# Kernel tuning notes

Measured on AMD Instinct MI355X. Metric: run time of the kernel, lower is better.

Reference implementation:

```python
import jax, jax.numpy as jnp
import numpy as np

B, H, W, C = 1, 56, 56, 96
DI = 192          # d_inner = ssm_ratio * hidden_dim
N  = 16           # d_state
DR = 6            # dt_rank = ceil(96/16)
K  = 4            # cross-scan directions
MH = 384          # mlp hidden = 4*C
L  = H * W


def _ln(x, g, b):
    m = x.mean(-1, keepdims=True)
    v = ((x - m) ** 2).mean(-1, keepdims=True)
    return (x - m) * jax.lax.rsqrt(v + 1e-5) * g + b


def setup_inputs() -> dict:
    key = jax.random.key(0)
    ks = jax.random.split(key, 12)
    r = lambda i, shape, s=0.02: jax.random.normal(ks[i], shape, jnp.float32) * s
    # S4D-real init for A_logs: log(1..N) tiled over K*DI channels
    A_logs = jnp.log(jnp.tile(jnp.arange(1, N + 1, dtype=jnp.float32)[None, :], (K * DI, 1)))
    return dict(
        x=jax.random.normal(ks[0], (B, H, W, C), jnp.float32),
        norm_g=jnp.ones((C,)), norm_b=jnp.zeros((C,)),
        in_proj_w=r(1, (C, 2 * DI)),
        conv_w=r(2, (3, 3, 1, DI)), conv_b=jnp.zeros((DI,)),
        x_proj_w=r(3, (K, DR + 2 * N, DI)),
        dt_projs_w=r(4, (K, DI, DR), 0.1), dt_projs_b=r(5, (K, DI), 0.1),
        A_logs=A_logs, Ds=jnp.ones((K * DI,)),
        out_norm_g=jnp.ones((DI,)), out_norm_b=jnp.zeros((DI,)),
        out_proj_w=r(6, (DI, C)),
        norm2_g=jnp.ones((C,)), norm2_b=jnp.zeros((C,)),
        fc1_w=r(7, (C, MH)), fc1_b=jnp.zeros((MH,)),
        fc2_w=r(8, (MH, C)), fc2_b=jnp.zeros((C,)),
    )


def _ss2d(x, in_proj_w, conv_w, conv_b, x_proj_w, dt_projs_w, dt_projs_b,
          A_logs, Ds, out_norm_g, out_norm_b, out_proj_w):
    xz = x @ in_proj_w                                  # (B,H,W,2*DI)
    xx, z = xz[..., :DI], xz[..., DI:]
    z = jax.nn.silu(z)
    xx = jax.lax.conv_general_dilated(
        xx, conv_w, (1, 1), 'SAME',
        dimension_numbers=('NHWC', 'HWIO', 'NHWC'),
        feature_group_count=DI) + conv_b               # depthwise 3x3
    xx = jax.nn.silu(xx)
    # cross-scan: row-major, col-major, and their reverses -> (B,K,DI,L)
    xd = jnp.transpose(xx, (0, 3, 1, 2)).reshape(B, DI, L)
    xt = jnp.transpose(xx, (0, 3, 2, 1)).reshape(B, DI, L)
    xs = jnp.stack([xd, xt, xd[..., ::-1], xt[..., ::-1]], 1)
    xdbl = jnp.einsum('bkdl,kcd->bkcl', xs, x_proj_w)
    dts, Bs, Cs = xdbl[:, :, :DR], xdbl[:, :, DR:DR + N], xdbl[:, :, DR + N:]
    dts = jnp.einsum('bkrl,kdr->bkdl', dts, dt_projs_w)
    dts = jax.nn.softplus(dts + dt_projs_b[None, :, :, None])      # (B,K,DI,L)
    A = -jnp.exp(A_logs).reshape(K, DI, N)
    # selective scan as first-order linear recurrence h_t = a_t*h_{t-1} + b_t
    a = jnp.exp(dts[..., None] * A[None, :, :, None, :])           # (B,K,DI,L,N)
    b = dts[..., None] * jnp.swapaxes(Bs, -1, -2)[:, :, None] * xs[..., None]
    def comb(c1, c2):
        a1, b1 = c1
        a2, b2 = c2
        return a1 * a2, a2 * b1 + b2
    _, hs = jax.lax.associative_scan(comb, (a, b), axis=3)         # (B,K,DI,L,N)
    ys = jnp.einsum('bkdln,bknl->bkdl', hs, Cs) + Ds.reshape(K, DI)[None, :, :, None] * xs
    # cross-merge: un-flip, un-transpose, sum the 4 directions
    yrow = ys[:, 0] + ys[:, 2, :, ::-1]
    ycol = ys[:, 1] + ys[:, 3, :, ::-1]
    y = yrow + jnp.transpose(ycol.reshape(B, DI, W, H), (0, 1, 3, 2)).reshape(B, DI, L)
    y = jnp.transpose(y.reshape(B, DI, H, W), (0, 2, 3, 1))        # (B,H,W,DI)
    y = _ln(y, out_norm_g, out_norm_b) * z
    return y @ out_proj_w


def reference(x, norm_g, norm_b, in_proj_w, conv_w, conv_b, x_proj_w,
              dt_projs_w, dt_projs_b, A_logs, Ds, out_norm_g, out_norm_b,
              out_proj_w, norm2_g, norm2_b, fc1_w, fc1_b, fc2_w, fc2_b):
    x = x + _ss2d(_ln(x, norm_g, norm_b), in_proj_w, conv_w, conv_b, x_proj_w,
                  dt_projs_w, dt_projs_b, A_logs, Ds, out_norm_g, out_norm_b, out_proj_w)
    h = _ln(x, norm2_g, norm2_b)
    x = x + (jax.nn.gelu(h @ fc1_w + fc1_b) @ fc2_w + fc2_b)
    return x
```

## Files before the change

kernel.cpp:

```cpp
#include <hip/hip_runtime.h>
#include <math.h>

constexpr int cH = 56, cW = 56, cC = 96, cDI = 192, cN = 16, cDR = 6, cK = 4, cMH = 384;
constexpr int cL = cH * cW;
constexpr int cNC = 196;
constexpr int cCH = 16;
constexpr float LOG2E = 1.44269504088896340736f;

__device__ __forceinline__ float fast_exp2(float x) { return __builtin_amdgcn_exp2f(x); }
__device__ __forceinline__ float siluf(float x) { return x / (1.f + expf(-x)); }
__device__ __forceinline__ float geluf(float x) {
    float x3 = x * x * x;
    return 0.5f * x * (1.f + tanhf(0.7978845608028654f * (x + 0.044715f * x3)));
}

__global__ void ln96_kernel(const float* __restrict__ x, const float* __restrict__ g,
                            const float* __restrict__ b, float* __restrict__ out, int M) {
    int wid = threadIdx.x >> 6;
    int lane = threadIdx.x & 63;
    int row = blockIdx.x * 4 + wid;
    if (row >= M) return;
    const float* xr = x + row * cC;
    float v0 = xr[lane];
    float v1 = (lane < cC - 64) ? xr[lane + 64] : 0.f;
    float s = v0 + v1;
    float sq = v0 * v0 + v1 * v1;
#pragma unroll
    for (int off = 32; off; off >>= 1) {
        s += __shfl_xor(s, off, 64);
        sq += __shfl_xor(sq, off, 64);
    }
    float m = s * (1.f / cC);
    float var = sq * (1.f / cC) - m * m;
    float rstd = rsqrtf(var + 1e-5f);
    out[row * cC + lane] = (v0 - m) * rstd * g[lane] + b[lane];
    if (lane < cC - 64)
        out[row * cC + lane + 64] = (v1 - m) * rstd * g[lane + 64] + b[lane + 64];
}

template <int ACT, bool HASB, bool HASR>
__global__ __launch_bounds__(256) void gemm_tile_kernel(
    const float* __restrict__ A, const float* __restrict__ B,
    const float* __restrict__ bias, const float* __restrict__ res,
    float* __restrict__ C, int M, int Nn, int Kk) {
    __shared__ float As[64][36];
    __shared__ float Bs[32][32];
    int tid = threadIdx.x;
    int tx = tid & 15;
    int ty = tid >> 4;
    int row0 = blockIdx.y * 64;
    int n0 = blockIdx.x * 32;
    float acc[4][2] = {{0.f, 0.f}, {0.f, 0.f}, {0.f, 0.f}, {0.f, 0.f}};
    int nt = Kk >> 5;
    for (int kt = 0; kt < nt; kt++) {
#pragma unroll
        for (int t = 0; t < 2; t++) {
            int f = tid + t * 256;
            int ar = f >> 3, ac = (f & 7) * 4;
            const float4 v = *reinterpret_cast<const float4*>(
                A + (size_t)(row0 + ar) * Kk + kt * 32 + ac);
            *reinterpret_cast<float4*>(&As[ar][ac]) = v;
        }
        {
            int br = tid >> 3, bc = (tid & 7) * 4;
            const float4 v = *reinterpret_cast<const float4*>(
                B + (size_t)(kt * 32 + br) * Nn + n0 + bc);
            *reinterpret_cast<float4*>(&Bs[br][bc]) = v;
        }
        __syncthreads();
#pragma unroll
        for (int k4 = 0; k4 < 8; k4++) {
            float4 a0 = *reinterpret_cast<float4*>(&As[ty * 4 + 0][k4 * 4]);
            float4 a1 = *reinterpret_cast<float4*>(&As[ty * 4 + 1][k4 * 4]);
            float4 a2 = *reinterpret_cast<float4*>(&As[ty * 4 + 2][k4 * 4]);
            float4 a3 = *reinterpret_cast<float4*>(&As[ty * 4 + 3][k4 * 4]);
            float2 b0 = *reinterpret_cast<float2*>(&Bs[k4 * 4 + 0][tx * 2]);
            float2 b1 = *reinterpret_cast<float2*>(&Bs[k4 * 4 + 1][tx * 2]);
            float2 b2 = *reinterpret_cast<float2*>(&Bs[k4 * 4 + 2][tx * 2]);
            float2 b3 = *reinterpret_cast<float2*>(&Bs[k4 * 4 + 3][tx * 2]);
            acc[0][0] = fmaf(a0.x, b0.x, acc[0][0]); acc[0][1] = fmaf(a0.x, b0.y, acc[0][1]);
            acc[1][0] = fmaf(a1.x, b0.x, acc[1][0]); acc[1][1] = fmaf(a1.x, b0.y, acc[1][1]);
            acc[2][0] = fmaf(a2.x, b0.x, acc[2][0]); acc[2][1] = fmaf(a2.x, b0.y, acc[2][1]);
            acc[3][0] = fmaf(a3.x, b0.x, acc[3][0]); acc[3][1] = fmaf(a3.x, b0.y, acc[3][1]);
            acc[0][0] = fmaf(a0.y, b1.x, acc[0][0]); acc[0][1] = fmaf(a0.y, b1.y, acc[0][1]);
            acc[1][0] = fmaf(a1.y, b1.x, acc[1][0]); acc[1][1] = fmaf(a1.y, b1.y, acc[1][1]);
            acc[2][0] = fmaf(a2.y, b1.x, acc[2][0]); acc[2][1] = fmaf(a2.y, b1.y, acc[2][1]);
            acc[3][0] = fmaf(a3.y, b1.x, acc[3][0]); acc[3][1] = fmaf(a3.y, b1.y, acc[3][1]);
            acc[0][0] = fmaf(a0.z, b2.x, acc[0][0]); acc[0][1] = fmaf(a0.z, b2.y, acc[0][1]);
            acc[1][0] = fmaf(a1.z, b2.x, acc[1][0]); acc[1][1] = fmaf(a1.z, b2.y, acc[1][1]);
            acc[2][0] = fmaf(a2.z, b2.x, acc[2][0]); acc[2][1] = fmaf(a2.z, b2.y, acc[2][1]);
            acc[3][0] = fmaf(a3.z, b2.x, acc[3][0]); acc[3][1] = fmaf(a3.z, b2.y, acc[3][1]);
            acc[0][0] = fmaf(a0.w, b3.x, acc[0][0]); acc[0][1] = fmaf(a0.w, b3.y, acc[0][1]);
            acc[1][0] = fmaf(a1.w, b3.x, acc[1][0]); acc[1][1] = fmaf(a1.w, b3.y, acc[1][1]);
            acc[2][0] = fmaf(a2.w, b3.x, acc[2][0]); acc[2][1] = fmaf(a2.w, b3.y, acc[2][1]);
            acc[3][0] = fmaf(a3.w, b3.x, acc[3][0]); acc[3][1] = fmaf(a3.w, b3.y, acc[3][1]);
        }
        __syncthreads();
    }
    int cc = n0 + tx * 2;
    float bx_ = 0.f, by_ = 0.f;
    if (HASB) { bx_ = bias[cc]; by_ = bias[cc + 1]; }
#pragma unroll
    for (int i = 0; i < 4; i++) {
        int rr = row0 + ty * 4 + i;
        float v0 = acc[i][0], v1 = acc[i][1];
        if (HASB) { v0 += bx_; v1 += by_; }
        if (ACT == 1) { v0 = geluf(v0); v1 = geluf(v1); }
        if (HASR) {
            const float2 r2 = *reinterpret_cast<const float2*>(res + (size_t)rr * Nn + cc);
            v0 += r2.x; v1 += r2.y;
        }
        float2 o; o.x = v0; o.y = v1;
        *reinterpret_cast<float2*>(C + (size_t)rr * Nn + cc) = o;
    }
}

__global__ void conv_silu_kernel(const float* __restrict__ xz, const float* __restrict__ cw,
                                 const float* __restrict__ cb, float* __restrict__ out) {
    int idx = blockIdx.x * 256 + threadIdx.x;
    if (idx >= cL * cDI) return;
    int d = idx % cDI;
    int l = idx / cDI;
    int h = l / cW, w = l % cW;
    float s = cb[d];
#pragma unroll
    for (int dh = 0; dh < 3; dh++) {
        int hh = h + dh - 1;
        if (hh < 0 || hh >= cH) continue;
#pragma unroll
        for (int dw = 0; dw < 3; dw++) {
            int w2 = w + dw - 1;
            if (w2 < 0 || w2 >= cW) continue;
            s = fmaf(xz[(size_t)(hh * cW + w2) * (2 * cDI) + d], cw[(dh * 3 + dw) * cDI + d], s);
        }
    }
    out[idx] = siluf(s);
}

__global__ void proj_kernel(const float* __restrict__ xconv, const float* __restrict__ xpw,
                            const float* __restrict__ dtw, const float* __restrict__ dtb,
                            float* __restrict__ dtT, float* __restrict__ Bsout,
                            float* __restrict__ Csout) {
    __shared__ float XS[16 * 193];
    __shared__ float DTS[6 * 16];
    __shared__ float DTW[cDI * cDR];
    int k = blockIdx.y;
    int p0 = blockIdx.x * 16;
    int tid = threadIdx.x;
    for (int i = tid; i < cDI * cDR; i += 256) DTW[i] = dtw[k * cDI * cDR + i];
    for (int idx = tid; idx < 16 * cDI; idx += 256) {
        int p = idx / cDI, d = idx % cDI;
        int j = p0 + p;
        int jj = (k >= 2) ? (cL - 1 - j) : j;
        int rrow = (k & 1) ? ((jj % cH) * cW + (jj / cH)) : jj;
        XS[p * 193 + d] = xconv[(size_t)rrow * cDI + d];
    }
    __syncthreads();
    for (int o = tid; o < 38 * 16; o += 256) {
        int c = o >> 4, p = o & 15;
        const float* wr = xpw + (size_t)(k * 38 + c) * cDI;
        const float* xr = XS + p * 193;
        float s = 0.f;
#pragma unroll 4
        for (int d = 0; d < cDI; d++) s = fmaf(wr[d], xr[d], s);
        if (c < 6) DTS[c * 16 + p] = s;
        else if (c < 22) Bsout[(size_t)(k * cL + p0 + p) * cN + (c - 6)] = s;
        else Csout[(size_t)(k * cL + p0 + p) * cN + (c - 22)] = s;
    }
    __syncthreads();
    for (int o = tid; o < cDI * 16; o += 256) {
        int d = o % cDI, p = o / cDI;
        float s = dtb[k * cDI + d];
#pragma unroll
        for (int r = 0; r < cDR; r++) s = fmaf(DTW[d * cDR + r], DTS[r * 16 + p], s);
        float sp = (s > 20.f) ? s : log1pf(expf(s));
        dtT[(size_t)(k * cL + p0 + p) * cDI + d] = sp;
    }
}

__device__ __forceinline__ void walker_init(int k, int j0, int& r, int& dr) {
    if (k == 0) { r = j0; dr = 1; }
    else if (k == 1) { r = (j0 % cH) * cW + (j0 / cH); dr = cW; }
    else if (k == 2) { r = cL - 1 - j0; dr = -1; }
    else { int jp = cL - 1 - j0; r = (jp % cH) * cW + (jp / cH); dr = -cW; }
}
__device__ __forceinline__ void walker_step(int& r, int dr) {
    r += dr;
    if (r >= cL) r -= cL - 1;
    else if (r < 0) r += cL - 1;
}

__global__ __launch_bounds__(192) void scan1_kernel(
    const float* __restrict__ dtT, const float* __restrict__ Bs,
    const float* __restrict__ xconv, const float* __restrict__ Alogs,
    float* __restrict__ carryP, float* __restrict__ carryH) {
    int c = blockIdx.x % cNC;
    int k = blockIdx.x / cNC;
    int d = threadIdx.x;
    int kd = k * cDI + d;
    int j0 = c * cCH;
    __shared__ float BS[cCH * cN];
    for (int i = threadIdx.x; i < cCH * cN; i += 192)
        BS[i] = Bs[(size_t)(k * cL + j0) * cN + i];
    float An2[cN];
#pragma unroll
    for (int n = 0; n < cN; n++)
        An2[n] = -fast_exp2(Alogs[kd * cN + n] * LOG2E) * LOG2E;
    int r, dr;
    walker_init(k, j0, r, dr);
    __syncthreads();
    float h[cN];
#pragma unroll
    for (int n = 0; n < cN; n++) h[n] = 0.f;
    float S = 0.f;
    const float* dtp = dtT + (size_t)(k * cL + j0) * cDI + d;
    for (int i = 0; i < cCH; i++) {
        float dt = dtp[(size_t)i * cDI];
        float xv = xconv[r * cDI + d];
        walker_step(r, dr);
        float dtx = dt * xv;
        S += dt;
        const float4 b0 = *reinterpret_cast<const float4*>(&BS[i * cN + 0]);
        const float4 b1 = *reinterpret_cast<const float4*>(&BS[i * cN + 4]);
        const float4 b2 = *reinterpret_cast<const float4*>(&BS[i * cN + 8]);
        const float4 b3 = *reinterpret_cast<const float4*>(&BS[i * cN + 12]);
        float bb[cN] = {b0.x, b0.y, b0.z, b0.w, b1.x, b1.y, b1.z, b1.w,
                        b2.x, b2.y, b2.z, b2.w, b3.x, b3.y, b3.z, b3.w};
#pragma unroll
        for (int n = 0; n < cN; n++) {
            float a = fast_exp2(An2[n] * dt);
            h[n] = fmaf(a, h[n], bb[n] * dtx);
        }
    }
    size_t cb = (size_t)(kd * cNC + c) * cN;
#pragma unroll
    for (int n = 0; n < cN; n++) {
        carryH[cb + n] = h[n];
        carryP[cb + n] = fast_exp2(An2[n] * S);
    }
}

__global__ void scan2_kernel(const float* __restrict__ carryP, const float* __restrict__ carryH,
                             float* __restrict__ hin) {
    int gid = blockIdx.x * 256 + threadIdx.x;
    if (gid >= cK * cDI * cN) return;
    int kd = gid / cN, n = gid % cN;
    float h = 0.f;
    for (int c = 0; c < cNC; c++) {
        size_t idxc = (size_t)(kd * cNC + c) * cN + n;
        hin[idxc] = h;
        h = fmaf(carryP[idxc], h, carryH[idxc]);
    }
}

__global__ __launch_bounds__(192) void scan3_kernel(
    const float* __restrict__ dtT, const float* __restrict__ Bs,
    const float* __restrict__ Cs, const float* __restrict__ xconv,
    const float* __restrict__ Alogs, const float* __restrict__ Ds,
    const float* __restrict__ hin, float* __restrict__ ysS) {
    int c = blockIdx.x % cNC;
    int k = blockIdx.x / cNC;
    int d = threadIdx.x;
    int kd = k * cDI + d;
    int j0 = c * cCH;
    __shared__ float BS[cCH * cN];
    __shared__ float CS[cCH * cN];
    for (int i = threadIdx.x; i < cCH * cN; i += 192) {
        BS[i] = Bs[(size_t)(k * cL + j0) * cN + i];
        CS[i] = Cs[(size_t)(k * cL + j0) * cN + i];
    }
    float An2[cN];
#pragma unroll
    for (int n = 0; n < cN; n++)
        An2[n] = -fast_exp2(Alogs[kd * cN + n] * LOG2E) * LOG2E;
    float Dv = Ds[kd];
    int r, dr;
    walker_init(k, j0, r, dr);
    float h[cN];
    size_t cb = (size_t)(kd * cNC + c) * cN;
#pragma unroll
    for (int n = 0; n < cN; n++) h[n] = hin[cb + n];
    __syncthreads();
    const float* dtp = dtT + (size_t)(k * cL + j0) * cDI + d;
    float* yp = ysS + (size_t)(k * cL + j0) * cDI + d;
    for (int i = 0; i < cCH; i++) {
        float dt = dtp[(size_t)i * cDI];
        float xv = xconv[r * cDI + d];
        walker_step(r, dr);
        float dtx = dt * xv;
        const float4 b0 = *reinterpret_cast<const float4*>(&BS[i * cN + 0]);
        const float4 b1 = *reinterpret_cast<const float4*>(&BS[i * cN + 4]);
        const float4 b2 = *reinterpret_cast<const float4*>(&BS[i * cN + 8]);
        const float4 b3 = *reinterpret_cast<const float4*>(&BS[i * cN + 12]);
        float bb[cN] = {b0.x, b0.y, b0.z, b0.w, b1.x, b1.y, b1.z, b1.w,
                        b2.x, b2.y, b2.z, b2.w, b3.x, b3.y, b3.z, b3.w};
        const float4 c0 = *reinterpret_cast<const float4*>(&CS[i * cN + 0]);
        const float4 c1 = *reinterpret_cast<const float4*>(&CS[i * cN + 4]);
        const float4 c2 = *reinterpret_cast<const float4*>(&CS[i * cN + 8]);
        const float4 c3 = *reinterpret_cast<const float4*>(&CS[i * cN + 12]);
        float cc[cN] = {c0.x, c0.y, c0.z, c0.w, c1.x, c1.y, c1.z, c1.w,
                        c2.x, c2.y, c2.z, c2.w, c3.x, c3.y, c3.z, c3.w};
        float y0 = 0.f, y1 = 0.f, y2 = 0.f, y3 = 0.f;
#pragma unroll
        for (int n = 0; n < cN; n += 4) {
            float a0 = fast_exp2(An2[n + 0] * dt);
            float a1 = fast_exp2(An2[n + 1] * dt);
            float a2 = fast_exp2(An2[n + 2] * dt);
            float a3 = fast_exp2(An2[n + 3] * dt);
            h[n + 0] = fmaf(a0, h[n + 0], bb[n + 0] * dtx);
            h[n + 1] = fmaf(a1, h[n + 1], bb[n + 1] * dtx);
            h[n + 2] = fmaf(a2, h[n + 2], bb[n + 2] * dtx);
            h[n + 3] = fmaf(a3, h[n + 3], bb[n + 3] * dtx);
            y0 = fmaf(h[n + 0], cc[n + 0], y0);
            y1 = fmaf(h[n + 1], cc[n + 1], y1);
            y2 = fmaf(h[n + 2], cc[n + 2], y2);
            y3 = fmaf(h[n + 3], cc[n + 3], y3);
        }
        yp[(size_t)i * cDI] = (y0 + y1) + (y2 + y3) + Dv * xv;
    }
}

__global__ void lnout_kernel(const float* __restrict__ ysS, const float* __restrict__ xz,
                             const float* __restrict__ g, const float* __restrict__ b,
                             float* __restrict__ ymul) {
    int wid = threadIdx.x >> 6, lane = threadIdx.x & 63;
    int l = blockIdx.x * 4 + wid;
    if (l >= cL) return;
    int h_ = l / cW, w_ = l % cW;
    int lc = w_ * cH + h_;
    float v[3];
    float s = 0.f, sq = 0.f;
#pragma unroll
    for (int j = 0; j < 3; j++) {
        int d = lane + j * 64;
        float t = ysS[(size_t)(0 * cL + l) * cDI + d] +
                  ysS[(size_t)(1 * cL + lc) * cDI + d] +
                  ysS[(size_t)(2 * cL + (cL - 1 - l)) * cDI + d] +
                  ysS[(size_t)(3 * cL + (cL - 1 - lc)) * cDI + d];
        v[j] = t;
        s += t;
        sq += t * t;
    }
#pragma unroll
    for (int off = 32; off; off >>= 1) {
        s += __shfl_xor(s, off, 64);
        sq += __shfl_xor(sq, off, 64);
    }
    float m = s * (1.f / cDI);
    float var = sq * (1.f / cDI) - m * m;
    float rstd = rsqrtf(var + 1e-5f);
#pragma unroll
    for (int j = 0; j < 3; j++) {
        int d = lane + j * 64;
        float z = xz[(size_t)l * (2 * cDI) + cDI + d];
        ymul[(size_t)l * cDI + d] = ((v[j] - m) * rstd * g[d] + b[d]) * siluf(z);
    }
}

extern "C" void kernel_launch(void* const* d_in, const int* in_sizes, int n_in,
                              void* d_out, int out_size, void* d_ws, size_t ws_size,
                              hipStream_t stream) {
    const float* x         = (const float*)d_in[0];
    const float* norm_g    = (const float*)d_in[1];
    const float* norm_b    = (const float*)d_in[2];
    const float* in_proj_w = (const float*)d_in[3];
    const float* conv_w    = (const float*)d_in[4];
    const float* conv_b    = (const float*)d_in[5];
    const float* x_proj_w  = (const float*)d_in[6];
    const float* dt_projs_w= (const float*)d_in[7];
    const float* dt_projs_b= (const float*)d_in[8];
    const float* A_logs    = (const float*)d_in[9];
    const float* Ds        = (const float*)d_in[10];
    const float* out_norm_g= (const float*)d_in[11];
    const float* out_norm_b= (const float*)d_in[12];
    const float* out_proj_w= (const float*)d_in[13];
    const float* norm2_g   = (const float*)d_in[14];
    const float* norm2_b   = (const float*)d_in[15];
    const float* fc1_w     = (const float*)d_in[16];
    const float* fc1_b     = (const float*)d_in[17];
    const float* fc2_w     = (const float*)d_in[18];
    const float* fc2_b     = (const float*)d_in[19];

    float* ws = (float*)d_ws;
    float* ln_buf = ws;
    float* xz     = ws + 301056;
    float* xconv  = ws + 1505280;
    float* dtT    = ws + 2107392;
    float* Bs     = ws + 4515840;
    float* Cs     = ws + 4716544;
    float* hin    = ws + 4917248;
    float* cP     = ws + 7325696;
    float* cHh    = ws + 9734144;
    float* ysS    = ws + 12142592;
    float* x1     = ws + 14551040;
    float* ymul   = xconv;
    float* hm     = xz;
    float* out    = (float*)d_out;

    ln96_kernel<<<cL / 4, 256, 0, stream>>>(x, norm_g, norm_b, ln_buf, cL);
    gemm_tile_kernel<0, false, false><<<dim3(384 / 32, cL / 64), 256, 0, stream>>>(
        ln_buf, in_proj_w, nullptr, nullptr, xz, cL, 2 * cDI, cC);
    conv_silu_kernel<<<(cL * cDI) / 256, 256, 0, stream>>>(xz, conv_w, conv_b, xconv);
    proj_kernel<<<dim3(cL / 16, cK), 256, 0, stream>>>(xconv, x_proj_w, dt_projs_w,
                                                       dt_projs_b, dtT, Bs, Cs);
    scan1_kernel<<<cK * cNC, 192, 0, stream>>>(dtT, Bs, xconv, A_logs, cP, cHh);
    scan2_kernel<<<(cK * cDI * cN + 255) / 256, 256, 0, stream>>>(cP, cHh, hin);
    scan3_kernel<<<cK * cNC, 192, 0, stream>>>(dtT, Bs, Cs, xconv, A_logs, Ds, hin, ysS);
    lnout_kernel<<<cL / 4, 256, 0, stream>>>(ysS, xz, out_norm_g, out_norm_b, ymul);
    gemm_tile_kernel<0, false, true><<<dim3(96 / 32, cL / 64), 256, 0, stream>>>(
        ymul, out_proj_w, nullptr, x, x1, cL, cC, cDI);
    ln96_kernel<<<cL / 4, 256, 0, stream>>>(x1, norm2_g, norm2_b, ln_buf, cL);
    gemm_tile_kernel<1, true, false><<<dim3(384 / 32, cL / 64), 256, 0, stream>>>(
        ln_buf, fc1_w, fc1_b, nullptr, hm, cL, cMH, cC);
    gemm_tile_kernel<0, true, true><<<dim3(96 / 32, cL / 64), 256, 0, stream>>>(
        hm, fc2_w, fc2_b, x1, out, cL, cC, cMH);
}
```

Before: 166.8 us.

## Fuse layernorms into GEMMs and double scan chunk length

Folds the two LayerNorm-96 passes into the following GEMM prologues, and fuses the cross-merge, out-norm and gating with the out_proj GEMM plus residual. This removes three kernel launches and the round trips through the intermediate ln and ymul buffers. The scan chunk count is halved and the chunk length doubled, which cuts the carry storage but leaves fewer blocks for the scan kernels. The fused GEMMs recompute LayerNorm statistics once per column tile, so that work is repeated 12 times for the 384-wide outputs.

```diff
diff --git a/kernel.cpp b/kernel.cpp
--- a/kernel.cpp
+++ b/kernel.cpp
@@ -3,8 +3,8 @@
 
 constexpr int cH = 56, cW = 56, cC = 96, cDI = 192, cN = 16, cDR = 6, cK = 4, cMH = 384;
 constexpr int cL = cH * cW;
-constexpr int cNC = 196;
-constexpr int cCH = 16;
+constexpr int cNC = 98;
+constexpr int cCH = 32;
 constexpr float LOG2E = 1.44269504088896340736f;
 
 __device__ __forceinline__ float fast_exp2(float x) { return __builtin_amdgcn_exp2f(x); }
@@ -14,28 +14,101 @@
     return 0.5f * x * (1.f + tanhf(0.7978845608028654f * (x + 0.044715f * x3)));
 }
 
-__global__ void ln96_kernel(const float* __restrict__ x, const float* __restrict__ g,
-                            const float* __restrict__ b, float* __restrict__ out, int M) {
-    int wid = threadIdx.x >> 6;
-    int lane = threadIdx.x & 63;
-    int row = blockIdx.x * 4 + wid;
-    if (row >= M) return;
-    const float* xr = x + row * cC;
-    float v0 = xr[lane];
-    float v1 = (lane < cC - 64) ? xr[lane + 64] : 0.f;
-    float s = v0 + v1;
-    float sq = v0 * v0 + v1 * v1;
-#pragma unroll
-    for (int off = 32; off; off >>= 1) {
-        s += __shfl_xor(s, off, 64);
-        sq += __shfl_xor(sq, off, 64);
-    }
-    float m = s * (1.f / cC);
-    float var = sq * (1.f / cC) - m * m;
-    float rstd = rsqrtf(var + 1e-5f);
-    out[row * cC + lane] = (v0 - m) * rstd * g[lane] + b[lane];
-    if (lane < cC - 64)
-        out[row * cC + lane + 64] = (v1 - m) * rstd * g[lane + 64] + b[lane + 64];
+template <int ACT, bool HASB>
+__global__ __launch_bounds__(256) void gemm_ln_tile(
+    const float* __restrict__ A, const float* __restrict__ g, const float* __restrict__ b,
+    const float* __restrict__ B, const float* __restrict__ bias,
+    float* __restrict__ C, int M, int Nn) {
+    __shared__ float As[64][100];
+    __shared__ float Bs2[32][32];
+    __shared__ float gB[96], bB[96], rowM[64], rowR[64];
+    int tid = threadIdx.x;
+    int row0 = blockIdx.y * 64;
+    int n0 = blockIdx.x * 32;
+    if (tid < 96) { gB[tid] = g[tid]; bB[tid] = b[tid]; }
+#pragma unroll
+    for (int t = 0; t < 6; t++) {
+        int f = tid + t * 256;
+        int ar = f / 24, ac4 = (f % 24) * 4;
+        const float4 v = *reinterpret_cast<const float4*>(A + (size_t)(row0 + ar) * 96 + ac4);
+        *reinterpret_cast<float4*>(&As[ar][ac4]) = v;
+    }
+    __syncthreads();
+    {
+        int row = tid >> 2, q = tid & 3;
+        float s = 0.f, sq = 0.f;
+#pragma unroll
+        for (int c = 0; c < 24; c++) {
+            float v = As[row][q * 24 + c];
+            s += v; sq += v * v;
+        }
+        s += __shfl_xor(s, 1); sq += __shfl_xor(sq, 1);
+        s += __shfl_xor(s, 2); sq += __shfl_xor(sq, 2);
+        if (q == 0) {
+            float m = s * (1.f / 96.f);
+            float var = sq * (1.f / 96.f) - m * m;
+            rowM[row] = m;
+            rowR[row] = rsqrtf(var + 1e-5f);
+        }
+    }
+    __syncthreads();
+    for (int i = tid; i < 64 * 96; i += 256) {
+        int r = i / 96, c = i % 96;
+        As[r][c] = (As[r][c] - rowM[r]) * rowR[r] * gB[c] + bB[c];
+    }
+    __syncthreads();
+    int tx = tid & 15, ty = tid >> 4;
+    float acc[4][2] = {{0.f, 0.f}, {0.f, 0.f}, {0.f, 0.f}, {0.f, 0.f}};
+#pragma unroll
+    for (int kt = 0; kt < 3; kt++) {
+        {
+            int br = tid >> 3, bc = (tid & 7) * 4;
+            const float4 v = *reinterpret_cast<const float4*>(
+                B + (size_t)(kt * 32 + br) * Nn + n0 + bc);
+            *reinterpret_cast<float4*>(&Bs2[br][bc]) = v;
+        }
+        __syncthreads();
+#pragma unroll
+        for (int k4 = 0; k4 < 8; k4++) {
+            float4 a0 = *reinterpret_cast<float4*>(&As[ty * 4 + 0][kt * 32 + k4 * 4]);
+            float4 a1 = *reinterpret_cast<float4*>(&As[ty * 4 + 1][kt * 32 + k4 * 4]);
+            float4 a2 = *reinterpret_cast<float4*>(&As[ty * 4 + 2][kt * 32 + k4 * 4]);
+            float4 a3 = *reinterpret_cast<float4*>(&As[ty * 4 + 3][kt * 32 + k4 * 4]);
+            float2 b0 = *reinterpret_cast<float2*>(&Bs2[k4 * 4 + 0][tx * 2]);
+            float2 b1 = *reinterpret_cast<float2*>(&Bs2[k4 * 4 + 1][tx * 2]);
+            float2 b2 = *reinterpret_cast<float2*>(&Bs2[k4 * 4 + 2][tx * 2]);
+            float2 b3 = *reinterpret_cast<float2*>(&Bs2[k4 * 4 + 3][tx * 2]);
+            acc[0][0] = fmaf(a0.x, b0.x, acc[0][0]); acc[0][1] = fmaf(a0.x, b0.y, acc[0][1]);
+            acc[1][0] = fmaf(a1.x, b0.x, acc[1][0]); acc[1][1] = fmaf(a1.x, b0.y, acc[1][1]);
+            acc[2][0] = fmaf(a2.x, b0.x, acc[2][0]); acc[2][1] = fmaf(a2.x, b0.y, acc[2][1]);
+            acc[3][0] = fmaf(a3.x, b0.x, acc[3][0]); acc[3][1] = fmaf(a3.x, b0.y, acc[3][1]);
+            acc[0][0] = fmaf(a0.y, b1.x, acc[0][0]); acc[0][1] = fmaf(a0.y, b1.y, acc[0][1]);
+            acc[1][0] = fmaf(a1.y, b1.x, acc[1][0]); acc[1][1] = fmaf(a1.y, b1.y, acc[1][1]);
+            acc[2][0] = fmaf(a2.y, b1.x, acc[2][0]); acc[2][1] = fmaf(a2.y, b1.y, acc[2][1]);
+            acc[3][0] = fmaf(a3.y, b1.x, acc[3][0]); acc[3][1] = fmaf(a3.y, b1.y, acc[3][1]);
+            acc[0][0] = fmaf(a0.z, b2.x, acc[0][0]); acc[0][1] = fmaf(a0.z, b2.y, acc[0][1]);
+            acc[1][0] = fmaf(a1.z, b2.x, acc[1][0]); acc[1][1] = fmaf(a1.z, b2.y, acc[1][1]);
+            acc[2][0] = fmaf(a2.z, b2.x, acc[2][0]); acc[2][1] = fmaf(a2.z, b2.y, acc[2][1]);
+            acc[3][0] = fmaf(a3.z, b2.x, acc[3][0]); acc[3][1] = fmaf(a3.z, b2.y, acc[3][1]);
+            acc[0][0] = fmaf(a0.w, b3.x, acc[0][0]); acc[0][1] = fmaf(a0.w, b3.y, acc[0][1]);
+            acc[1][0] = fmaf(a1.w, b3.x, acc[1][0]); acc[1][1] = fmaf(a1.w, b3.y, acc[1][1]);
+            acc[2][0] = fmaf(a2.w, b3.x, acc[2][0]); acc[2][1] = fmaf(a2.w, b3.y, acc[2][1]);
+            acc[3][0] = fmaf(a3.w, b3.x, acc[3][0]); acc[3][1] = fmaf(a3.w, b3.y, acc[3][1]);
+        }
+        __syncthreads();
+    }
+    int cc = n0 + tx * 2;
+    float bx_ = 0.f, by_ = 0.f;
+    if (HASB) { bx_ = bias[cc]; by_ = bias[cc + 1]; }
+#pragma unroll
+    for (int i = 0; i < 4; i++) {
+        int rr = row0 + ty * 4 + i;
+        float v0 = acc[i][0], v1 = acc[i][1];
+        if (HASB) { v0 += bx_; v1 += by_; }
+        if (ACT == 1) { v0 = geluf(v0); v1 = geluf(v1); }
+        float2 o; o.x = v0; o.y = v1;
+        *reinterpret_cast<float2*>(C + (size_t)rr * Nn + cc) = o;
+    }
 }
 
 template <int ACT, bool HASB, bool HASR>
@@ -115,6 +188,96 @@
     }
 }
 
+__global__ __launch_bounds__(256) void lnout_gemm_kernel(
+    const float* __restrict__ ysS, const float* __restrict__ xz,
+    const float* __restrict__ g, const float* __restrict__ b,
+    const float* __restrict__ W, const float* __restrict__ resx,
+    float* __restrict__ C) {
+    __shared__ float As[16][196];
+    __shared__ float Bs[32][96];
+    __shared__ float gB[192], bB[192], rowM[16], rowR[16];
+    int tid = threadIdx.x;
+    int row0 = blockIdx.x * 16;
+    if (tid < 192) { gB[tid] = g[tid]; bB[tid] = b[tid]; }
+#pragma unroll
+    for (int t = 0; t < 3; t++) {
+        int f = tid + t * 256;
+        int rr = f / 48, d4 = (f % 48) * 4;
+        int l = row0 + rr;
+        int h_ = l / cW, w_ = l % cW;
+        int lc = w_ * cH + h_;
+        const float4 y0 = *reinterpret_cast<const float4*>(ysS + (size_t)(0 * cL + l) * cDI + d4);
+        const float4 y1 = *reinterpret_cast<const float4*>(ysS + (size_t)(1 * cL + lc) * cDI + d4);
+        const float4 y2 = *reinterpret_cast<const float4*>(ysS + (size_t)(2 * cL + (cL - 1 - l)) * cDI + d4);
+        const float4 y3 = *reinterpret_cast<const float4*>(ysS + (size_t)(3 * cL + (cL - 1 - lc)) * cDI + d4);
+        float4 o;
+        o.x = y0.x + y1.x + y2.x + y3.x;
+        o.y = y0.y + y1.y + y2.y + y3.y;
+        o.z = y0.z + y1.z + y2.z + y3.z;
+        o.w = y0.w + y1.w + y2.w + y3.w;
+        *reinterpret_cast<float4*>(&As[rr][d4]) = o;
+    }
+    __syncthreads();
+    {
+        int row = tid >> 4, seg = tid & 15;
+        float s = 0.f, sq = 0.f;
+#pragma unroll
+        for (int c = 0; c < 12; c++) {
+            float v = As[row][seg * 12 + c];
+            s += v; sq += v * v;
+        }
+        s += __shfl_xor(s, 1); sq += __shfl_xor(sq, 1);
+        s += __shfl_xor(s, 2); sq += __shfl_xor(sq, 2);
+        s += __shfl_xor(s, 4); sq += __shfl_xor(sq, 4);
+        s += __shfl_xor(s, 8); sq += __shfl_xor(sq, 8);
+        if (seg == 0) {
+            float m = s * (1.f / 192.f);
+            float var = sq * (1.f / 192.f) - m * m;
+            rowM[row] = m;
+            rowR[row] = rsqrtf(var + 1e-5f);
+        }
+    }
+    __syncthreads();
+    for (int i = tid; i < 16 * 192; i += 256) {
+        int rr = i / 192, c = i % 192;
+        int l = row0 + rr;
+        float z = xz[(size_t)l * (2 * cDI) + cDI + c];
+        As[rr][c] = ((As[rr][c] - rowM[rr]) * rowR[rr] * gB[c] + bB[c]) * siluf(z);
+    }
+    __syncthreads();
+    int tx = tid & 31, ty = tid >> 5;
+    int c0 = tx * 3;
+    float acc[2][3] = {{0.f, 0.f, 0.f}, {0.f, 0.f, 0.f}};
+#pragma unroll
+    for (int kt = 0; kt < 6; kt++) {
+        for (int i2 = tid; i2 < 32 * 96; i2 += 256) {
+            int kk = i2 / 96, c = i2 % 96;
+            Bs[kk][c] = W[(size_t)(kt * 32 + kk) * 96 + c];
+        }
+        __syncthreads();
+#pragma unroll
+        for (int k = 0; k < 32; k++) {
+            float a0 = As[ty][kt * 32 + k];
+            float a1 = As[ty + 8][kt * 32 + k];
+            float b0 = Bs[k][c0], b1 = Bs[k][c0 + 1], b2 = Bs[k][c0 + 2];
+            acc[0][0] = fmaf(a0, b0, acc[0][0]);
+            acc[0][1] = fmaf(a0, b1, acc[0][1]);
+            acc[0][2] = fmaf(a0, b2, acc[0][2]);
+            acc[1][0] = fmaf(a1, b0, acc[1][0]);
+            acc[1][1] = fmaf(a1, b1, acc[1][1]);
+            acc[1][2] = fmaf(a1, b2, acc[1][2]);
+        }
+        __syncthreads();
+    }
+#pragma unroll
+    for (int i = 0; i < 2; i++) {
+        int rr = row0 + ty + 8 * i;
+#pragma unroll
+        for (int j = 0; j < 3; j++)
+            C[(size_t)rr * 96 + c0 + j] = acc[i][j] + resx[(size_t)rr * 96 + c0 + j];
+    }
+}
+
 __global__ void conv_silu_kernel(const float* __restrict__ xz, const float* __restrict__ cw,
                                  const float* __restrict__ cb, float* __restrict__ out) {
     int idx = blockIdx.x * 256 + threadIdx.x;
@@ -317,43 +480,6 @@
             y3 = fmaf(h[n + 3], cc[n + 3], y3);
         }
         yp[(size_t)i * cDI] = (y0 + y1) + (y2 + y3) + Dv * xv;
-    }
-}
-
-__global__ void lnout_kernel(const float* __restrict__ ysS, const float* __restrict__ xz,
-                             const float* __restrict__ g, const float* __restrict__ b,
-                             float* __restrict__ ymul) {
-    int wid = threadIdx.x >> 6, lane = threadIdx.x & 63;
-    int l = blockIdx.x * 4 + wid;
-    if (l >= cL) return;
-    int h_ = l / cW, w_ = l % cW;
-    int lc = w_ * cH + h_;
-    float v[3];
-    float s = 0.f, sq = 0.f;
-#pragma unroll
-    for (int j = 0; j < 3; j++) {
-        int d = lane + j * 64;
-        float t = ysS[(size_t)(0 * cL + l) * cDI + d] +
-                  ysS[(size_t)(1 * cL + lc) * cDI + d] +
-                  ysS[(size_t)(2 * cL + (cL - 1 - l)) * cDI + d] +
-                  ysS[(size_t)(3 * cL + (cL - 1 - lc)) * cDI + d];
-        v[j] = t;
-        s += t;
-        sq += t * t;
-    }
-#pragma unroll
-    for (int off = 32; off; off >>= 1) {
-        s += __shfl_xor(s, off, 64);
-        sq += __shfl_xor(sq, off, 64);
-    }
-    float m = s * (1.f / cDI);
-    float var = sq * (1.f / cDI) - m * m;
-    float rstd = rsqrtf(var + 1e-5f);
-#pragma unroll
-    for (int j = 0; j < 3; j++) {
-        int d = lane + j * 64;
-        float z = xz[(size_t)l * (2 * cDI) + cDI + d];
-        ymul[(size_t)l * cDI + d] = ((v[j] - m) * rstd * g[d] + b[d]) * siluf(z);
     }
 }
 
@@ -382,36 +508,31 @@
     const float* fc2_b     = (const float*)d_in[19];
 
     float* ws = (float*)d_ws;
-    float* ln_buf = ws;
-    float* xz     = ws + 301056;
-    float* xconv  = ws + 1505280;
-    float* dtT    = ws + 2107392;
-    float* Bs     = ws + 4515840;
-    float* Cs     = ws + 4716544;
-    float* hin    = ws + 4917248;
-    float* cP     = ws + 7325696;
-    float* cHh    = ws + 9734144;
-    float* ysS    = ws + 12142592;
-    float* x1     = ws + 14551040;
-    float* ymul   = xconv;
+    float* xz     = ws;
+    float* xconv  = ws + 1204224;
+    float* dtT    = ws + 1806336;
+    float* Bs     = ws + 4214784;
+    float* Cs     = ws + 4415488;
+    float* hin    = ws + 4616192;
+    float* cP     = ws + 5820416;
+    float* cHh    = ws + 7024640;
+    float* ysS    = ws + 8228864;
+    float* x1     = ws + 10637312;
     float* hm     = xz;
     float* out    = (float*)d_out;
 
-    ln96_kernel<<<cL / 4, 256, 0, stream>>>(x, norm_g, norm_b, ln_buf, cL);
-    gemm_tile_kernel<0, false, false><<<dim3(384 / 32, cL / 64), 256, 0, stream>>>(
-        ln_buf, in_proj_w, nullptr, nullptr, xz, cL, 2 * cDI, cC);
+    gemm_ln_tile<0, false><<<dim3(384 / 32, cL / 64), 256, 0, stream>>>(
+        x, norm_g, norm_b, in_proj_w, nullptr, xz, cL, 2 * cDI);
     conv_silu_kernel<<<(cL * cDI) / 256, 256, 0, stream>>>(xz, conv_w, conv_b, xconv);
     proj_kernel<<<dim3(cL / 16, cK), 256, 0, stream>>>(xconv, x_proj_w, dt_projs_w,
                                                        dt_projs_b, dtT, Bs, Cs);
     scan1_kernel<<<cK * cNC, 192, 0, stream>>>(dtT, Bs, xconv, A_logs, cP, cHh);
     scan2_kernel<<<(cK * cDI * cN + 255) / 256, 256, 0, stream>>>(cP, cHh, hin);
     scan3_kernel<<<cK * cNC, 192, 0, stream>>>(dtT, Bs, Cs, xconv, A_logs, Ds, hin, ysS);
-    lnout_kernel<<<cL / 4, 256, 0, stream>>>(ysS, xz, out_norm_g, out_norm_b, ymul);
-    gemm_tile_kernel<0, false, true><<<dim3(96 / 32, cL / 64), 256, 0, stream>>>(
-        ymul, out_proj_w, nullptr, x, x1, cL, cC, cDI);
-    ln96_kernel<<<cL / 4, 256, 0, stream>>>(x1, norm2_g, norm2_b, ln_buf, cL);
-    gemm_tile_kernel<1, true, false><<<dim3(384 / 32, cL / 64), 256, 0, stream>>>(
-        ln_buf, fc1_w, fc1_b, nullptr, hm, cL, cMH, cC);
+    lnout_gemm_kernel<<<cL / 16, 256, 0, stream>>>(ysS, xz, out_norm_g, out_norm_b,
+                                                   out_proj_w, x, x1);
+    gemm_ln_tile<1, true><<<dim3(384 / 32, cL / 64), 256, 0, stream>>>(
+        x1, norm2_g, norm2_b, fc1_w, fc1_b, hm, cL, cMH);
     gemm_tile_kernel<0, true, true><<<dim3(96 / 32, cL / 64), 256, 0, stream>>>(
         hm, fc2_w, fc2_b, x1, out, cL, cC, cMH);
 }
```

After: 201.2 us. 20.6% more time.
